# Kernel tuning notes

Hardware: AMD Instinct MI355X
Metric: run time of the kernel (lower is better)

The kernel has to match this reference:

```python
import jax, jax.numpy as jnp
import numpy as np

TAU = 0.01          # gumbel_softmax temperature
EPS = 1e-7          # tf.keras.backend.epsilon()
DEPTH = 5
N_NODES = 2 ** DEPTH - 1   # 31 internal nodes
N_LEAVES = 2 ** DEPTH      # 32 leaves


def _build_route():
    # route[l, node + dir*N_NODES] = 1 along the root-to-leaf path of leaf l
    # (same structure old_route_to_new_route produces for a perfect tree)
    route = np.zeros((N_LEAVES, 2 * N_NODES), dtype=np.float32)
    for l in range(N_LEAVES):
        node = 0
        for d in range(DEPTH):
            bit = (l >> (DEPTH - 1 - d)) & 1  # 0 = left, 1 = right
            route[l, node + bit * N_NODES] = 1.0
            node = 2 * node + 1 + bit
    return route


def setup_inputs() -> dict:
    B, F, T = 32768, 128, 100
    key = jax.random.key(0)
    k1, k2, k3, k4 = jax.random.split(key, 4)
    x = jax.random.normal(k1, (B, F), dtype=jnp.float32)
    kernel = jax.random.normal(k2, (T, F, N_NODES), dtype=jnp.float32) * 0.1
    bias = jax.random.normal(k3, (T, N_NODES), dtype=jnp.float32) * 0.1
    leaf = jax.random.normal(k4, (T, N_LEAVES), dtype=jnp.float32)
    route = jnp.asarray(_build_route())  # [L, 2N], shared tree topology
    return {"x": x, "kernel": kernel, "bias": bias, "leaf": leaf, "route": route}


def reference(x, kernel, bias, leaf, route):
    # NodeLayer: matmul(x, concat([K, -K], 1)) + concat([b, -b], 0)
    h = jnp.einsum("bf,tfn->btn", x, kernel) + bias          # [B, T, N]
    h2 = jnp.concatenate([h, -h], axis=-1)                   # [B, T, 2N]
    # activation1: log(clip(sigmoid(clip(h/tau, -32, 32)), eps, 1))
    a1 = jnp.log(jnp.clip(jax.nn.sigmoid(jnp.clip(h2 / TAU, -32.0, 32.0)), EPS, 1.0))
    # route aggregation: sum log-probs along each root->leaf path
    r = jnp.einsum("btm,lm->btl", a1, route)                 # [B, T, L]
    # activation2: exp(clip(., -32, 0)) -> leaf routing probabilities
    probs = jnp.exp(jnp.clip(r, -32.0, 0.0))
    # weight leaf values by route probabilities, sum over leaves and trees
    return jnp.einsum("btl,tl->b", probs, leaf)              # [B] raw GBM output
```

## Files before the change

kernel.cpp:

```cpp
#include <hip/hip_runtime.h>

typedef _Float16 f16x8  __attribute__((ext_vector_type(8)));
typedef float    f32x16 __attribute__((ext_vector_type(16)));
typedef float    f32x4  __attribute__((ext_vector_type(4)));

#define NTREES  100
#define WAVES   8
#define NCH     13
#define BM      64
#define KS      9
#define TSTRIDE (KS * 512)
#define NSCALE  (-144.269504088896f)

__device__ __forceinline__ int node_of_row(int sr, float& sg) {
  const int h   = (sr >> 2) & 1;
  const int reg = (sr & 3) + ((sr >> 3) << 2);
  sg = 1.0f;
  if (reg == 0) { if (h) sg = -1.0f; return 0; }
  if (reg == 1) return 1 + h;
  if (reg < 4)  return 1 + 2 * h + reg;
  if (reg < 8)  return 3 + 4 * h + reg;
  return 7 + 8 * h + reg;
}

__device__ __forceinline__ float exp2_fast(float v) {
#if __has_builtin(__builtin_amdgcn_exp2f)
  return __builtin_amdgcn_exp2f(v);
#else
  return exp2f(v);
#endif
}

__device__ __forceinline__ float sigl(float zn) {
  float e = exp2_fast(zn);
  return __builtin_amdgcn_rcpf(1.0f + e);
}

__global__ void prep_b(const float* __restrict__ kern, const float* __restrict__ bias,
                       unsigned short* __restrict__ bws) {
  __shared__ float kt[128][32];
  __shared__ float bs[32];
  const int t = blockIdx.x, tid = threadIdx.x;
  const float* src = kern + (size_t)t * (128 * 31);
  for (int i = tid; i < 128 * 32; i += 256) {
    const int f = i >> 5, sr_ = i & 31;
    float sg; const int g = node_of_row(sr_, sg);
    kt[f][sr_] = src[f * 31 + g] * (NSCALE * sg);
  }
  if (tid < 32) {
    float sg; const int g = node_of_row(tid, sg);
    bs[tid] = bias[t * 31 + g] * (NSCALE * sg);
  }
  __syncthreads();
  unsigned short* dst = bws + (size_t)t * TSTRIDE;
  for (int s = tid; s < KS * 64; s += 256) {
    const int ks = s >> 6, lane = s & 63;
    const int row = lane & 31;
    const int k0 = ks * 16 + ((lane >> 5) << 3);
    f16x8 o;
    if (ks < 8) {
      #pragma unroll
      for (int j = 0; j < 8; ++j) o[j] = (_Float16)kt[k0 + j][row];
    } else {
      #pragma unroll
      for (int j = 0; j < 8; ++j) o[j] = (_Float16)0.0f;
      if (lane < 32) o[0] = (_Float16)bs[row];
    }
    *(f16x8*)(dst + s * 8) = o;
  }
}

__device__ __forceinline__ float half_eval(const f32x16& a, const f32x4& L0,
                                           const f32x4& L1, const f32x4& L2,
                                           const f32x4& L3) {
  float sl, sr;
  const float c0 = sigl(a[0]);
  sl = sigl(a[1]); sr = 1.0f - sl;
  const float a0 = c0 * sl, a1 = c0 * sr;
  sl = sigl(a[2]); sr = 1.0f - sl;
  const float b0 = a0 * sl, b1 = a0 * sr;
  sl = sigl(a[3]); sr = 1.0f - sl;
  const float b2 = a1 * sl, b3 = a1 * sr;
  float cum[8];
  sl = sigl(a[4]); sr = 1.0f - sl; cum[0] = b0 * sl; cum[1] = b0 * sr;
  sl = sigl(a[5]); sr = 1.0f - sl; cum[2] = b1 * sl; cum[3] = b1 * sr;
  sl = sigl(a[6]); sr = 1.0f - sl; cum[4] = b2 * sl; cum[5] = b2 * sr;
  sl = sigl(a[7]); sr = 1.0f - sl; cum[6] = b3 * sl; cum[7] = b3 * sr;
  float s = 0.0f;
  s = fmaf(cum[0], fmaf(sigl(a[8]),  L0[0] - L0[1], L0[1]), s);
  s = fmaf(cum[1], fmaf(sigl(a[9]),  L0[2] - L0[3], L0[3]), s);
  s = fmaf(cum[2], fmaf(sigl(a[10]), L1[0] - L1[1], L1[1]), s);
  s = fmaf(cum[3], fmaf(sigl(a[11]), L1[2] - L1[3], L1[3]), s);
  s = fmaf(cum[4], fmaf(sigl(a[12]), L2[0] - L2[1], L2[1]), s);
  s = fmaf(cum[5], fmaf(sigl(a[13]), L2[2] - L2[3], L2[3]), s);
  s = fmaf(cum[6], fmaf(sigl(a[14]), L3[0] - L3[1], L3[1]), s);
  s = fmaf(cum[7], fmaf(sigl(a[15]), L3[2] - L3[3], L3[3]), s);
  return s;
}

__global__ __launch_bounds__(512, 4) void gbm_main(
    const float* __restrict__ x,
    const unsigned short* __restrict__ bws,
    const float* __restrict__ leaf,
    float* __restrict__ out)
{
  __shared__ __align__(16) unsigned char lds[2 * KS * 64 * 16];
  float* red = (float*)lds;

  const int tid  = threadIdx.x;
  const int lane = tid & 63;
  const int w    = tid >> 6;
  const int rowbase = blockIdx.x * BM;

  #pragma unroll
  for (int T = 0; T < 2; ++T)
    for (int s = tid; s < KS * 64; s += 512) {
      const int ks = s >> 6, l = s & 63;
      f16x8 h8;
      if (ks < 8) {
        const int xrow = (l & 31) + T * 32;
        const int k0 = ks * 16 + ((l >> 5) << 3);
        const float* px = x + (size_t)(rowbase + xrow) * 128 + k0;
        float4 v0 = *(const float4*)px;
        float4 v1 = *(const float4*)(px + 4);
        h8[0] = (_Float16)v0.x; h8[1] = (_Float16)v0.y;
        h8[2] = (_Float16)v0.z; h8[3] = (_Float16)v0.w;
        h8[4] = (_Float16)v1.x; h8[5] = (_Float16)v1.y;
        h8[6] = (_Float16)v1.z; h8[7] = (_Float16)v1.w;
      } else {
        #pragma unroll
        for (int j = 0; j < 8; ++j) h8[j] = (_Float16)0.0f;
        if (l < 32) h8[0] = (_Float16)1.0f;
      }
      *(f16x8*)(lds + T * (KS * 64 * 16) + s * 16) = h8;
    }

  f16x8 br[KS];
  {
    const unsigned short* bt = bws + (size_t)w * TSTRIDE;
    #pragma unroll
    for (int i = 0; i < KS; ++i)
      br[i] = *(const f16x8*)(bt + (size_t)i * 512 + lane * 8);
  }

  __syncthreads();

  const int h = lane >> 5;
  float outAcc0 = 0.0f, outAcc1 = 0.0f;

  for (int c = 0; c < NCH; ++c) {
    const int tree = c * WAVES + w;
    const bool act = tree < NTREES;

    f32x16 acc0 = {}, acc1 = {};
    if (act) {
      __builtin_amdgcn_s_setprio(1);
      #pragma unroll
      for (int ks = 0; ks < KS; ++ks) {
        f16x8 bx0 = *(const f16x8*)(lds + (ks * 64 + lane) * 16);
        f16x8 bx1 = *(const f16x8*)(lds + KS * 64 * 16 + (ks * 64 + lane) * 16);
        acc0 = __builtin_amdgcn_mfma_f32_32x32x16_f16(br[ks], bx0, acc0, 0, 0, 0);
        acc1 = __builtin_amdgcn_mfma_f32_32x32x16_f16(br[ks], bx1, acc1, 0, 0, 0);
      }
      __builtin_amdgcn_s_setprio(0);
    }

    if ((c + 1) * WAVES + w < NTREES) {
      const unsigned short* nb = bws + (size_t)((c + 1) * WAVES + w) * TSTRIDE;
      #pragma unroll
      for (int i = 0; i < KS; ++i)
        br[i] = *(const f16x8*)(nb + (size_t)i * 512 + lane * 8);
    }

    if (act) {
      const float* lp = leaf + (size_t)tree * 32 + (h << 4);
      f32x4 L0 = *(const f32x4*)lp;
      f32x4 L1 = *(const f32x4*)(lp + 4);
      f32x4 L2 = *(const f32x4*)(lp + 8);
      f32x4 L3 = *(const f32x4*)(lp + 12);

      outAcc0 += half_eval(acc0, L0, L1, L2, L3);
      outAcc1 += half_eval(acc1, L0, L1, L2, L3);
    }
  }

  __syncthreads();
  red[tid] = outAcc0;
  red[512 + tid] = outAcc1;
  __syncthreads();
  if (tid < BM) {
    const int tile = tid >> 5, r = tid & 31;
    float s = 0.0f;
    #pragma unroll
    for (int j = 0; j < 16; ++j)
      s += red[tile * 512 + j * 32 + r];
    out[rowbase + tid] = s;
  }
}

extern "C" void kernel_launch(void* const* d_in, const int* in_sizes, int n_in,
                              void* d_out, int out_size, void* d_ws, size_t ws_size,
                              hipStream_t stream) {
  const float* x    = (const float*)d_in[0];
  const float* kern = (const float*)d_in[1];
  const float* bias = (const float*)d_in[2];
  const float* leaf = (const float*)d_in[3];

  unsigned short* bws = (unsigned short*)d_ws;

  prep_b<<<NTREES, 256, 0, stream>>>(kern, bias, bws);
  gbm_main<<<32768 / BM, 512, 0, stream>>>(x, bws, leaf, (float*)d_out);
}
```

Baseline: 52.35 us.

## Evaluate tree bottom-up with numerator/denominator form and shrink blocks to four waves

```diff
diff --git a/kernel.cpp b/kernel.cpp
--- a/kernel.cpp
+++ b/kernel.cpp
@@ -5,8 +5,8 @@
 typedef float    f32x4  __attribute__((ext_vector_type(4)));
 
 #define NTREES  100
-#define WAVES   8
-#define NCH     13
+#define WAVES   4
+#define NCH     25
 #define BM      64
 #define KS      9
 #define TSTRIDE (KS * 512)
@@ -31,9 +31,54 @@
 #endif
 }
 
-__device__ __forceinline__ float sigl(float zn) {
-  float e = exp2_fast(zn);
-  return __builtin_amdgcn_rcpf(1.0f + e);
+__device__ __forceinline__ void nd_leaf(float ai, float Ll, float Lr,
+                                        float& n, float& d) {
+  const float emag = exp2_fast(-__builtin_fabsf(ai));
+  const bool  sw   = ai > 0.0f;
+  const float ta   = sw ? Ll : Lr;
+  const float tb   = sw ? Lr : Ll;
+  n = fmaf(emag, ta, tb);
+  d = 1.0f + emag;
+}
+__device__ __forceinline__ void nd_int(float ai, float nl, float dl,
+                                       float nr, float dr, float& n, float& d) {
+  const float emag = exp2_fast(-__builtin_fabsf(ai));
+  const float t0 = nl * dr, t1 = nr * dl;
+  const bool  sw = ai > 0.0f;
+  const float ta = sw ? t0 : t1;
+  const float tb = sw ? t1 : t0;
+  n = fmaf(emag, ta, tb);
+  const float dd = dl * dr;
+  d = fmaf(emag, dd, dd);
+}
+
+__device__ __forceinline__ float half_eval(const f32x16& a, const f32x4& L0,
+                                           const f32x4& L1, const f32x4& L2,
+                                           const f32x4& L3, float outAcc) {
+  float n0,d0,n1,d1,n2,d2,n3,d3,n4,d4,n5,d5,n6,d6,n7,d7;
+  nd_leaf(a[8],  L0[0], L0[1], n0, d0);
+  nd_leaf(a[9],  L0[2], L0[3], n1, d1);
+  nd_leaf(a[10], L1[0], L1[1], n2, d2);
+  nd_leaf(a[11], L1[2], L1[3], n3, d3);
+  nd_leaf(a[12], L2[0], L2[1], n4, d4);
+  nd_leaf(a[13], L2[2], L2[3], n5, d5);
+  nd_leaf(a[14], L3[0], L3[1], n6, d6);
+  nd_leaf(a[15], L3[2], L3[3], n7, d7);
+  float p0,q0,p1,q1,p2,q2,p3,q3;
+  nd_int(a[4], n0, d0, n1, d1, p0, q0);
+  nd_int(a[5], n2, d2, n3, d3, p1, q1);
+  nd_int(a[6], n4, d4, n5, d5, p2, q2);
+  nd_int(a[7], n6, d6, n7, d7, p3, q3);
+  float u0,v0,u1,v1;
+  nd_int(a[2], p0, q0, p1, q1, u0, v0);
+  nd_int(a[3], p2, q2, p3, q3, u1, v1);
+  float nf, df;
+  nd_int(a[1], u0, v0, u1, v1, nf, df);
+  const float emag0 = exp2_fast(-__builtin_fabsf(a[0]));
+  const float dfin  = fmaf(emag0, df, df);
+  const float nsc   = nf * emag0;
+  const float nfin  = (a[0] > 0.0f) ? nsc : nf;
+  return fmaf(nfin, __builtin_amdgcn_rcpf(dfin), outAcc);
 }
 
 __global__ void prep_b(const float* __restrict__ kern, const float* __restrict__ bias,
@@ -42,7 +87,7 @@
   __shared__ float bs[32];
   const int t = blockIdx.x, tid = threadIdx.x;
   const float* src = kern + (size_t)t * (128 * 31);
-  for (int i = tid; i < 128 * 32; i += 256) {
+  for (int i = tid; i < 128 * 32; i += 512) {
     const int f = i >> 5, sr_ = i & 31;
     float sg; const int g = node_of_row(sr_, sg);
     kt[f][sr_] = src[f * 31 + g] * (NSCALE * sg);
@@ -53,7 +98,7 @@
   }
   __syncthreads();
   unsigned short* dst = bws + (size_t)t * TSTRIDE;
-  for (int s = tid; s < KS * 64; s += 256) {
+  for (int s = tid; s < KS * 64; s += 512) {
     const int ks = s >> 6, lane = s & 63;
     const int row = lane & 31;
     const int k0 = ks * 16 + ((lane >> 5) << 3);
@@ -70,41 +115,13 @@
   }
 }
 
-__device__ __forceinline__ float half_eval(const f32x16& a, const f32x4& L0,
-                                           const f32x4& L1, const f32x4& L2,
-                                           const f32x4& L3) {
-  float sl, sr;
-  const float c0 = sigl(a[0]);
-  sl = sigl(a[1]); sr = 1.0f - sl;
-  const float a0 = c0 * sl, a1 = c0 * sr;
-  sl = sigl(a[2]); sr = 1.0f - sl;
-  const float b0 = a0 * sl, b1 = a0 * sr;
-  sl = sigl(a[3]); sr = 1.0f - sl;
-  const float b2 = a1 * sl, b3 = a1 * sr;
-  float cum[8];
-  sl = sigl(a[4]); sr = 1.0f - sl; cum[0] = b0 * sl; cum[1] = b0 * sr;
-  sl = sigl(a[5]); sr = 1.0f - sl; cum[2] = b1 * sl; cum[3] = b1 * sr;
-  sl = sigl(a[6]); sr = 1.0f - sl; cum[4] = b2 * sl; cum[5] = b2 * sr;
-  sl = sigl(a[7]); sr = 1.0f - sl; cum[6] = b3 * sl; cum[7] = b3 * sr;
-  float s = 0.0f;
-  s = fmaf(cum[0], fmaf(sigl(a[8]),  L0[0] - L0[1], L0[1]), s);
-  s = fmaf(cum[1], fmaf(sigl(a[9]),  L0[2] - L0[3], L0[3]), s);
-  s = fmaf(cum[2], fmaf(sigl(a[10]), L1[0] - L1[1], L1[1]), s);
-  s = fmaf(cum[3], fmaf(sigl(a[11]), L1[2] - L1[3], L1[3]), s);
-  s = fmaf(cum[4], fmaf(sigl(a[12]), L2[0] - L2[1], L2[1]), s);
-  s = fmaf(cum[5], fmaf(sigl(a[13]), L2[2] - L2[3], L2[3]), s);
-  s = fmaf(cum[6], fmaf(sigl(a[14]), L3[0] - L3[1], L3[1]), s);
-  s = fmaf(cum[7], fmaf(sigl(a[15]), L3[2] - L3[3], L3[3]), s);
-  return s;
-}
-
-__global__ __launch_bounds__(512, 4) void gbm_main(
+__global__ __launch_bounds__(256, 3) void gbm_main(
     const float* __restrict__ x,
     const unsigned short* __restrict__ bws,
     const float* __restrict__ leaf,
     float* __restrict__ out)
 {
-  __shared__ __align__(16) unsigned char lds[2 * KS * 64 * 16];
+  __shared__ __align__(16) unsigned char lds[2 * 8 * 64 * 16];
   float* red = (float*)lds;
 
   const int tid  = threadIdx.x;
@@ -114,26 +131,33 @@
 
   #pragma unroll
   for (int T = 0; T < 2; ++T)
-    for (int s = tid; s < KS * 64; s += 512) {
+    for (int s = tid; s < 8 * 64; s += 256) {
       const int ks = s >> 6, l = s & 63;
+      const int xrow = (l & 31) + T * 32;
+      const int k0 = ks * 16 + ((l >> 5) << 3);
+      const float* px = x + (size_t)(rowbase + xrow) * 128 + k0;
+      float4 v0 = *(const float4*)px;
+      float4 v1 = *(const float4*)(px + 4);
       f16x8 h8;
-      if (ks < 8) {
-        const int xrow = (l & 31) + T * 32;
-        const int k0 = ks * 16 + ((l >> 5) << 3);
-        const float* px = x + (size_t)(rowbase + xrow) * 128 + k0;
-        float4 v0 = *(const float4*)px;
-        float4 v1 = *(const float4*)(px + 4);
-        h8[0] = (_Float16)v0.x; h8[1] = (_Float16)v0.y;
-        h8[2] = (_Float16)v0.z; h8[3] = (_Float16)v0.w;
-        h8[4] = (_Float16)v1.x; h8[5] = (_Float16)v1.y;
-        h8[6] = (_Float16)v1.z; h8[7] = (_Float16)v1.w;
-      } else {
-        #pragma unroll
-        for (int j = 0; j < 8; ++j) h8[j] = (_Float16)0.0f;
-        if (l < 32) h8[0] = (_Float16)1.0f;
-      }
-      *(f16x8*)(lds + T * (KS * 64 * 16) + s * 16) = h8;
+      h8[0] = (_Float16)v0.x; h8[1] = (_Float16)v0.y;
+      h8[2] = (_Float16)v0.z; h8[3] = (_Float16)v0.w;
+      h8[4] = (_Float16)v1.x; h8[5] = (_Float16)v1.y;
+      h8[6] = (_Float16)v1.z; h8[7] = (_Float16)v1.w;
+      *(f16x8*)(lds + T * 8192 + s * 16) = h8;
     }
+  __syncthreads();
+
+  f16x8 bx[2][8];
+  #pragma unroll
+  for (int T = 0; T < 2; ++T)
+    #pragma unroll
+    for (int ks = 0; ks < 8; ++ks)
+      bx[T][ks] = *(const f16x8*)(lds + T * 8192 + (ks * 64 + lane) * 16);
+
+  f16x8 bxb;
+  #pragma unroll
+  for (int j = 0; j < 8; ++j) bxb[j] = (_Float16)0.0f;
+  if (lane < 32) bxb[0] = (_Float16)1.0f;
 
   f16x8 br[KS];
   {
@@ -143,57 +167,56 @@
       br[i] = *(const f16x8*)(bt + (size_t)i * 512 + lane * 8);
   }
 
-  __syncthreads();
-
   const int h = lane >> 5;
   float outAcc0 = 0.0f, outAcc1 = 0.0f;
 
   for (int c = 0; c < NCH; ++c) {
     const int tree = c * WAVES + w;
-    const bool act = tree < NTREES;
-
-    f32x16 acc0 = {}, acc1 = {};
-    if (act) {
-      __builtin_amdgcn_s_setprio(1);
-      #pragma unroll
-      for (int ks = 0; ks < KS; ++ks) {
-        f16x8 bx0 = *(const f16x8*)(lds + (ks * 64 + lane) * 16);
-        f16x8 bx1 = *(const f16x8*)(lds + KS * 64 * 16 + (ks * 64 + lane) * 16);
-        acc0 = __builtin_amdgcn_mfma_f32_32x32x16_f16(br[ks], bx0, acc0, 0, 0, 0);
-        acc1 = __builtin_amdgcn_mfma_f32_32x32x16_f16(br[ks], bx1, acc1, 0, 0, 0);
-      }
-      __builtin_amdgcn_s_setprio(0);
-    }
-
-    if ((c + 1) * WAVES + w < NTREES) {
+
+    const float* lp = leaf + (size_t)tree * 32 + (h << 4);
+    f32x4 L0 = *(const f32x4*)lp;
+    f32x4 L1 = *(const f32x4*)(lp + 4);
+    f32x4 L2 = *(const f32x4*)(lp + 8);
+    f32x4 L3 = *(const f32x4*)(lp + 12);
+
+    f32x16 a0 = {};
+    __builtin_amdgcn_s_setprio(1);
+    #pragma unroll
+    for (int ks = 0; ks < 8; ++ks)
+      a0 = __builtin_amdgcn_mfma_f32_32x32x16_f16(br[ks], bx[0][ks], a0, 0, 0, 0);
+    a0 = __builtin_amdgcn_mfma_f32_32x32x16_f16(br[8], bxb, a0, 0, 0, 0);
+    __builtin_amdgcn_s_setprio(0);
+    outAcc0 = half_eval(a0, L0, L1, L2, L3, outAcc0);
+
+    f32x16 a1 = {};
+    __builtin_amdgcn_s_setprio(1);
+    #pragma unroll
+    for (int ks = 0; ks < 8; ++ks)
+      a1 = __builtin_amdgcn_mfma_f32_32x32x16_f16(br[ks], bx[1][ks], a1, 0, 0, 0);
+    a1 = __builtin_amdgcn_mfma_f32_32x32x16_f16(br[8], bxb, a1, 0, 0, 0);
+    __builtin_amdgcn_s_setprio(0);
+
+    if (c + 1 < NCH) {
       const unsigned short* nb = bws + (size_t)((c + 1) * WAVES + w) * TSTRIDE;
       #pragma unroll
       for (int i = 0; i < KS; ++i)
         br[i] = *(const f16x8*)(nb + (size_t)i * 512 + lane * 8);
     }
 
-    if (act) {
-      const float* lp = leaf + (size_t)tree * 32 + (h << 4);
-      f32x4 L0 = *(const f32x4*)lp;
-      f32x4 L1 = *(const f32x4*)(lp + 4);
-      f32x4 L2 = *(const f32x4*)(lp + 8);
-      f32x4 L3 = *(const f32x4*)(lp + 12);
-
-      outAcc0 += half_eval(acc0, L0, L1, L2, L3);
-      outAcc1 += half_eval(acc1, L0, L1, L2, L3);
-    }
+    outAcc1 = half_eval(a1, L0, L1, L2, L3, outAcc1);
   }
 
   __syncthreads();
   red[tid] = outAcc0;
-  red[512 + tid] = outAcc1;
+  red[256 + tid] = outAcc1;
   __syncthreads();
   if (tid < BM) {
     const int tile = tid >> 5, r = tid & 31;
+    const float* rb = red + tile * 256 + r;
     float s = 0.0f;
     #pragma unroll
-    for (int j = 0; j < 16; ++j)
-      s += red[tile * 512 + j * 32 + r];
+    for (int j = 0; j < 8; ++j)
+      s += rb[((j >> 1) << 6) + ((j & 1) << 5)];
     out[rowbase + tid] = s;
   }
 }
@@ -208,6 +231,6 @@
 
   unsigned short* bws = (unsigned short*)d_ws;
 
-  prep_b<<<NTREES, 256, 0, stream>>>(kern, bias, bws);
-  gbm_main<<<32768 / BM, 512, 0, stream>>>(x, bws, leaf, (float*)d_out);
-}
+  prep_b<<<NTREES, 512, 0, stream>>>(kern, bias, bws);
+  gbm_main<<<32768 / BM, 256, 0, stream>>>(x, bws, leaf, (float*)d_out);
+}
```

After: 59.47 us. 1.14x slower.
